# Optimization experiments

Measured on AMD Instinct MI355X. Metric: run time of the kernel, lower is better.

## Reference

```python
import jax, jax.numpy as jnp
import numpy as np
from jax import lax


def _lstm(x, W_ih, W_hh, b_ih, b_hh, return_seq):
    """PyTorch-compatible single-layer LSTM, batch_first, zero init state.
    W_ih: [4H, D], W_hh: [4H, H], gate order (i, f, g, o).
    Returns [B, T, H] if return_seq else final hidden [B, H]."""
    B, T, _ = x.shape
    H = W_hh.shape[1]
    # Precompute input contribution for all timesteps: [B, T, 4H]
    xg = jnp.einsum('btd,gd->btg', x, W_ih) + b_ih + b_hh
    h0 = jnp.zeros((B, H), x.dtype)
    c0 = jnp.zeros((B, H), x.dtype)

    def step(carry, xt):
        h, c = carry
        g = xt + h @ W_hh.T  # [B, 4H]
        i, f, gg, o = jnp.split(g, 4, axis=-1)
        i = jax.nn.sigmoid(i)
        f = jax.nn.sigmoid(f)
        gg = jnp.tanh(gg)
        o = jax.nn.sigmoid(o)
        c = f * c + i * gg
        h = o * jnp.tanh(c)
        return (h, c), (h if return_seq else None)

    (hT, _), ys = lax.scan(step, (h0, c0), jnp.swapaxes(xg, 0, 1))
    if return_seq:
        return jnp.swapaxes(ys, 0, 1)  # [B, T, H]
    return hT


def setup_inputs() -> dict:
    key = jax.random.key(0)
    ks = jax.random.split(key, 12)
    B, T, D = 2048, 512, 64
    H1, H2 = 16, 4
    s = 0.1
    return {
        'x': jax.random.normal(ks[0], (B, T, D), jnp.float32),
        'W_ih1': jax.random.normal(ks[1], (4 * H1, D), jnp.float32) * s,
        'W_hh1': jax.random.normal(ks[2], (4 * H1, H1), jnp.float32) * s,
        'b_ih1': jax.random.normal(ks[3], (4 * H1,), jnp.float32) * s,
        'b_hh1': jax.random.normal(ks[4], (4 * H1,), jnp.float32) * s,
        'W_ih2': jax.random.normal(ks[5], (4 * H2, H1), jnp.float32) * s,
        'W_hh2': jax.random.normal(ks[6], (4 * H2, H2), jnp.float32) * s,
        'b_ih2': jax.random.normal(ks[7], (4 * H2,), jnp.float32) * s,
        'b_hh2': jax.random.normal(ks[8], (4 * H2,), jnp.float32) * s,
        'W_fc': jax.random.normal(ks[9], (D, H2), jnp.float32) * s,
        'b_fc': jax.random.normal(ks[10], (D,), jnp.float32) * s,
    }


def reference(x, W_ih1, W_hh1, b_ih1, b_hh1, W_ih2, W_hh2, b_ih2, b_hh2, W_fc, b_fc):
    y = _lstm(x, W_ih1, W_hh1, b_ih1, b_hh1, return_seq=True)  # [B, T, H1]
    y = jax.nn.relu(y)
    # Only the last timestep of lstm2 is used -> return final hidden state.
    y_last = _lstm(y, W_ih2, W_hh2, b_ih2, b_hh2, return_seq=False)  # [B, H2]
    out = y_last @ W_fc.T + b_fc  # [B, D]
    return jax.nn.sigmoid(out)
```

## Files before the change

kernel.cpp:

```cpp
#include <hip/hip_runtime.h>
#include <hip/hip_bf16.h>

#define T_ALL 512
#define TB 16
#define NB (T_ALL / TB)
#define LOG2E 1.44269504088896f
#define XSTR 68

typedef __attribute__((ext_vector_type(8))) short bf16x8;
typedef __attribute__((ext_vector_type(4))) float f32x4;

#define DPPF(v, CTRL) __uint_as_float((unsigned)__builtin_amdgcn_update_dpp(0, (int)__float_as_uint(v), (CTRL), 0xF, 0xF, true))
#define SWZF(v, PAT)  __uint_as_float((unsigned)__builtin_amdgcn_ds_swizzle((int)__float_as_uint(v), (PAT)))
#define BPERM(a, v)   __uint_as_float((unsigned)__builtin_amdgcn_ds_bpermute((a), (int)__float_as_uint(v)))

__device__ __forceinline__ unsigned pack2bf16(float a, float b) {
    unsigned ua = __float_as_uint(a), ub = __float_as_uint(b);
    ua += 0x7FFFu + ((ua >> 16) & 1u);
    ub += 0x7FFFu + ((ub >> 16) & 1u);
    return (ua >> 16) | (ub & 0xFFFF0000u);
}
__device__ __forceinline__ bf16x8 make_frag(float4 lo, float4 hi) {
    union { unsigned u[4]; bf16x8 v; } r;
    r.u[0] = pack2bf16(lo.x, lo.y);
    r.u[1] = pack2bf16(lo.z, lo.w);
    r.u[2] = pack2bf16(hi.x, hi.y);
    r.u[3] = pack2bf16(hi.z, hi.w);
    return r.v;
}
__device__ __forceinline__ float4 scale4(float4 v, float s) {
    return make_float4(v.x * s, v.y * s, v.z * s, v.w * s);
}
__device__ __forceinline__ float2 pkfma(float2 a, float2 b, float2 c) {
    return make_float2(fmaf(a.x, b.x, c.x), fmaf(a.y, b.y, c.y));
}
__device__ __forceinline__ float tanh_c(float c) {
    return fmaf(2.0f, __builtin_amdgcn_rcpf(
        1.0f + __builtin_amdgcn_exp2f(-2.0f * LOG2E * c)), -1.0f);
}
__device__ __forceinline__ float fsigm(float x) {
    return __builtin_amdgcn_rcpf(1.0f + __builtin_amdgcn_exp2f(-LOG2E * x));
}

__global__ __launch_bounds__(128, 4)
void lstm_fused_v8(const float* __restrict__ x,
        const float* __restrict__ Wih1, const float* __restrict__ Whh1,
        const float* __restrict__ bih1, const float* __restrict__ bhh1,
        const float* __restrict__ Wih2, const float* __restrict__ Whh2,
        const float* __restrict__ bih2, const float* __restrict__ bhh2,
        const float* __restrict__ Wfc,  const float* __restrict__ bfc,
        float* __restrict__ out)
{
    __shared__ __align__(16) float xgl[2][TB * XSTR];
    __shared__ __align__(16) float h1l[2][TB][16];

    const int tid = threadIdx.x;
    const int wid = tid >> 6;
    const int lane = tid & 63;
    const size_t b = blockIdx.x;

    const int tl = lane & 15;
    const int kh = lane >> 4;
    const int T1 = lane & 3;
    const int j1 = lane >> 2;

    const float aA1 = (T1 == 2) ? 2.0f : 1.0f, aB1 = (T1 == 2) ? -1.0f : 0.0f;

    bf16x8 wb[4][2];
    float bias1[4];
#pragma unroll
    for (int n = 0; n < 4; ++n) {
        const float scn = (n == 2) ? 2.0f * LOG2E : LOG2E;
#pragma unroll
        for (int kk = 0; kk < 2; ++kk) {
            const float* wp = Wih1 + (size_t)(n * 16 + tl) * 64 + kk * 32 + kh * 8;
            wb[n][kk] = make_frag(scale4(*(const float4*)wp, scn),
                                  scale4(*(const float4*)(wp + 4), scn));
        }
        bias1[n] = (bih1[n * 16 + tl] + bhh1[n * 16 + tl]) * scn;
    }

    float2 wrA0, wrA1, wrB0, wrB1, wrC0, wrC1, wrD0, wrD1;
    {
        const float sA = (T1 == 2) ? 2.0f * LOG2E : LOG2E;
        const float sB = ((T1 ^ 2) == 2) ? 2.0f * LOG2E : LOG2E;
        const float sC = ((T1 ^ 1) == 2) ? 2.0f * LOG2E : LOG2E;
        const float sD = ((T1 ^ 3) == 2) ? 2.0f * LOG2E : LOG2E;
        const float4 wa  = scale4(*(const float4*)(Whh1 + ((T1    ) * 16 + j1) * 16 + 4 * T1), sA);
        const float4 wbv = scale4(*(const float4*)(Whh1 + ((T1 ^ 2) * 16 + j1) * 16 + 4 * T1), sB);
        const float4 wc  = scale4(*(const float4*)(Whh1 + ((T1 ^ 1) * 16 + j1) * 16 + 4 * T1), sC);
        const float4 wd  = scale4(*(const float4*)(Whh1 + ((T1 ^ 3) * 16 + j1) * 16 + 4 * T1), sD);
        wrA0 = make_float2(wa.x, wa.y);   wrA1 = make_float2(wa.z, wa.w);
        wrB0 = make_float2(wbv.x, wbv.y); wrB1 = make_float2(wbv.z, wbv.w);
        wrC0 = make_float2(wc.x, wc.y);   wrC1 = make_float2(wc.z, wc.w);
        wrD0 = make_float2(wd.x, wd.y);   wrD1 = make_float2(wd.z, wd.w);
    }

    const int m2 = lane >> 4;
    const int T2 = (lane >> 2) & 3;
    const int s2 = lane & 3;
    const int row2 = T2 * 4 + m2;
    const float sc2 = (T2 == 2) ? 2.0f * LOG2E : LOG2E;
    const float aA2 = (T2 == 2) ? 2.0f : 1.0f, aB2 = (T2 == 2) ? -1.0f : 0.0f;
    const float4 w2q = scale4(*(const float4*)(Wih2 + row2 * 16 + 4 * s2), sc2);
    const float2 w2a = make_float2(w2q.x, w2q.y);
    const float2 w2b = make_float2(w2q.z, w2q.w);
    const float w2h = Whh2[row2 * 4 + s2] * sc2;
    const float bias2l = (s2 == 0) ? (bih2[row2] + bhh2[row2]) * sc2 : 0.0f;
    const float4 wfc = *(const float4*)(Wfc + lane * 4);
    const float bfcv = bfc[lane];

    const int ag0 = (16 * T1 + 0)  << 2;
    const int ag1 = (16 * T1 + 4)  << 2;
    const int ag2 = (16 * T1 + 8)  << 2;
    const int ag3 = (16 * T1 + 12) << 2;
    const int ahs = s2 << 6;
    const int gidx = T1 * 16 + j1;

    float c1r = 0.f, h1r = 0.f;
    float c2r = 0.f, h2v = 0.f, h2s = 0.f;

    const float* xb = x + b * (size_t)(T_ALL * 64);
    float4 xpf[4];
    const float2 zero2 = make_float2(0.f, 0.f);

#define LOADX(CH) do { \
    const float* _src = xb + (size_t)(CH) * (TB * 64); \
    _Pragma("unroll") \
    for (int _kk = 0; _kk < 2; ++_kk) \
        _Pragma("unroll") \
        for (int _hf = 0; _hf < 2; ++_hf) \
            xpf[_kk * 2 + _hf] = *(const float4*)(_src + tl * 64 + _kk * 32 + kh * 8 + _hf * 4); \
} while (0)

#define MFMA_XG(BUF) do { \
    bf16x8 _a0 = make_frag(xpf[0], xpf[1]); \
    bf16x8 _a1 = make_frag(xpf[2], xpf[3]); \
    _Pragma("unroll") \
    for (int _n = 0; _n < 4; ++_n) { \
        f32x4 _acc = {bias1[_n], bias1[_n], bias1[_n], bias1[_n]}; \
        _acc = __builtin_amdgcn_mfma_f32_16x16x32_bf16(_a0, wb[_n][0], _acc, 0, 0, 0); \
        _acc = __builtin_amdgcn_mfma_f32_16x16x32_bf16(_a1, wb[_n][1], _acc, 0, 0, 0); \
        _Pragma("unroll") \
        for (int _r = 0; _r < 4; ++_r) \
            xgl[BUF][(kh * 4 + _r) * XSTR + _n * 16 + tl] = _acc[_r]; \
    } \
} while (0)

#define STEP1(XU) do { \
    const float _g0 = BPERM(ag0, h1r); \
    const float _g1 = BPERM(ag1, h1r); \
    const float _g2 = BPERM(ag2, h1r); \
    const float _g3 = BPERM(ag3, h1r); \
    const float2 _g01 = make_float2(_g0, _g1); \
    const float2 _g23 = make_float2(_g2, _g3); \
    float2 _aA = pkfma(wrA0, _g01, make_float2((XU), 0.f)); _aA = pkfma(wrA1, _g23, _aA); \
    float2 _aB = pkfma(wrB0, _g01, zero2); _aB = pkfma(wrB1, _g23, _aB); \
    float2 _aC = pkfma(wrC0, _g01, zero2); _aC = pkfma(wrC1, _g23, _aC); \
    float2 _aD = pkfma(wrD0, _g01, zero2); _aD = pkfma(wrD1, _g23, _aD); \
    const float _sA = _aA.x + _aA.y, _sB2 = _aB.x + _aB.y; \
    const float _sC = _aC.x + _aC.y, _sD = _aD.x + _aD.y; \
    const float _u0 = _sA + DPPF(_sC, 0xB1); \
    const float _u1 = _sB2 + DPPF(_sD, 0xB1); \
    const float _pre = _u0 + DPPF(_u1, 0x4E); \
    const float _s1 = __builtin_amdgcn_rcpf(1.0f + __builtin_amdgcn_exp2f(-_pre)); \
    const float _act = fmaf(aA1, _s1, aB1); \
    const float _fv = DPPF(_act, 0x55); \
    const float _gv = DPPF(_act, 0xAA); \
    const float _ov = DPPF(_act, 0xFF); \
    c1r = fmaf(_fv, c1r, _act * _gv);         \
    h1r = _ov * tanh_c(c1r);                  \
} while (0)

#define LSTM2_STEP(RG, TT) do { \
    const float4 _rq = *(const float4*)&h1l[RG][TT][4 * s2]; \
    const float2 _r01 = make_float2(fmaxf(_rq.x, 0.f), fmaxf(_rq.y, 0.f)); \
    const float2 _r23 = make_float2(fmaxf(_rq.z, 0.f), fmaxf(_rq.w, 0.f)); \
    float2 _a2 = pkfma(w2a, _r01, make_float2(bias2l, w2h * h2s)); \
    _a2 = pkfma(w2b, _r23, _a2); \
    float _p2 = _a2.x + _a2.y; \
    _p2 += DPPF(_p2, 0xB1); \
    _p2 += DPPF(_p2, 0x4E); \
    const float _act2 = fmaf(aA2, \
        __builtin_amdgcn_rcpf(1.0f + __builtin_amdgcn_exp2f(-_p2)), aB2); \
    const float _fv2 = SWZF(_act2, 0x101F); \
    const float _gv2 = SWZF(_act2, 0x201F); \
    const float _ov2 = SWZF(_act2, 0x301F); \
    c2r = fmaf(_fv2, c2r, _act2 * _gv2);      \
    h2v = _ov2 * tanh_c(c2r); \
    h2s = BPERM(ahs, h2v); \
} while (0)

    if (wid == 1) {
        LOADX(0);
        MFMA_XG(0);
        LOADX(1);
    }
    __syncthreads();

    for (int c = 0; c < NB; ++c) {
        if (wid == 0) {
            const float* xrow = &xgl[c & 1][0];
            const int rg = c & 1;
#pragma unroll
            for (int tt = 0; tt < TB; ++tt) {
                const float xu = xrow[tt * XSTR + gidx];
                STEP1(xu);
                if (T1 == 0) h1l[rg][tt][j1] = h1r;
            }
        } else {
            if (c + 1 < NB) {
                bf16x8 a0s = make_frag(xpf[0], xpf[1]);
                bf16x8 a1s = make_frag(xpf[2], xpf[3]);
                if (c + 2 < NB) LOADX(c + 2);
#pragma unroll
                for (int n = 0; n < 4; ++n) {
                    f32x4 acc = {bias1[n], bias1[n], bias1[n], bias1[n]};
                    acc = __builtin_amdgcn_mfma_f32_16x16x32_bf16(a0s, wb[n][0], acc, 0, 0, 0);
                    acc = __builtin_amdgcn_mfma_f32_16x16x32_bf16(a1s, wb[n][1], acc, 0, 0, 0);
#pragma unroll
                    for (int r = 0; r < 4; ++r)
                        xgl[(c + 1) & 1][(kh * 4 + r) * XSTR + n * 16 + tl] = acc[r];
                }
            }
            if (c >= 1) {
                const int rg = (c - 1) & 1;
#pragma unroll
                for (int tt = 0; tt < TB; ++tt)
                    LSTM2_STEP(rg, tt);
            }
        }
        __syncthreads();
    }

    if (wid == 1) {
        const int rg = (NB - 1) & 1;
#pragma unroll
        for (int tt = 0; tt < TB; ++tt)
            LSTM2_STEP(rg, tt);

        const float hq0 = __shfl(h2v, 0);
        const float hq1 = __shfl(h2v, 16);
        const float hq2 = __shfl(h2v, 32);
        const float hq3 = __shfl(h2v, 48);
        float accf = bfcv;
        accf = fmaf(wfc.x, hq0, accf);
        accf = fmaf(wfc.y, hq1, accf);
        accf = fmaf(wfc.z, hq2, accf);
        accf = fmaf(wfc.w, hq3, accf);
        out[b * 64 + lane] = fsigm(accf);
    }
#undef LOADX
#undef MFMA_XG
#undef STEP1
#undef LSTM2_STEP
}

extern "C" void kernel_launch(void* const* d_in, const int* in_sizes, int n_in,
                              void* d_out, int out_size, void* d_ws, size_t ws_size,
                              hipStream_t stream) {
    const float* x    = (const float*)d_in[0];
    const float* Wih1 = (const float*)d_in[1];
    const float* Whh1 = (const float*)d_in[2];
    const float* bih1 = (const float*)d_in[3];
    const float* bhh1 = (const float*)d_in[4];
    const float* Wih2 = (const float*)d_in[5];
    const float* Whh2 = (const float*)d_in[6];
    const float* bih2 = (const float*)d_in[7];
    const float* bhh2 = (const float*)d_in[8];
    const float* Wfc  = (const float*)d_in[9];
    const float* bfc  = (const float*)d_in[10];
    float* out = (float*)d_out;

    lstm_fused_v8<<<dim3(2048), dim3(128), 0, stream>>>(
        x, Wih1, Whh1, bih1, bhh1, Wih2, Whh2, bih2, bhh2, Wfc, bfc, out);
}
```

Before: 161.3 us.

## Batch LSTM2 input projection per chunk with MFMA, trim recurrent critical path

The layer-2 input projection (ReLU(h1) times Wih2 plus bias) moves out of the per-timestep loop. Each 16-step chunk now computes it with one bf16 MFMA into a shared buffer, so each LSTM2 step only does the recurrent term plus a shared-memory load. The layer-1 step adds the precomputed input term after the DPP reductions, taking it off the dependent FMA chain. The bf16 packing switches from round-to-nearest-even to a cheaper add-and-perm rounding, and layer-2 input weights and activations are now rounded to bf16, which costs some precision.

```diff
diff --git a/kernel.cpp b/kernel.cpp
--- a/kernel.cpp
+++ b/kernel.cpp
@@ -14,25 +14,30 @@
 #define SWZF(v, PAT)  __uint_as_float((unsigned)__builtin_amdgcn_ds_swizzle((int)__float_as_uint(v), (PAT)))
 #define BPERM(a, v)   __uint_as_float((unsigned)__builtin_amdgcn_ds_bpermute((a), (int)__float_as_uint(v)))
 
-__device__ __forceinline__ unsigned pack2bf16(float a, float b) {
-    unsigned ua = __float_as_uint(a), ub = __float_as_uint(b);
-    ua += 0x7FFFu + ((ua >> 16) & 1u);
-    ub += 0x7FFFu + ((ub >> 16) & 1u);
-    return (ua >> 16) | (ub & 0xFFFF0000u);
+__device__ __forceinline__ unsigned pack2fast(float a, float b) {
+    const unsigned ua = __float_as_uint(a) + 0x8000u;
+    const unsigned ub = __float_as_uint(b) + 0x8000u;
+    return __builtin_amdgcn_perm(ub, ua, 0x07060302u);
 }
 __device__ __forceinline__ bf16x8 make_frag(float4 lo, float4 hi) {
     union { unsigned u[4]; bf16x8 v; } r;
-    r.u[0] = pack2bf16(lo.x, lo.y);
-    r.u[1] = pack2bf16(lo.z, lo.w);
-    r.u[2] = pack2bf16(hi.x, hi.y);
-    r.u[3] = pack2bf16(hi.z, hi.w);
+    r.u[0] = pack2fast(lo.x, lo.y);
+    r.u[1] = pack2fast(lo.z, lo.w);
+    r.u[2] = pack2fast(hi.x, hi.y);
+    r.u[3] = pack2fast(hi.z, hi.w);
     return r.v;
 }
 __device__ __forceinline__ float4 scale4(float4 v, float s) {
     return make_float4(v.x * s, v.y * s, v.z * s, v.w * s);
 }
+__device__ __forceinline__ float4 relu4(float4 v) {
+    return make_float4(fmaxf(v.x, 0.f), fmaxf(v.y, 0.f), fmaxf(v.z, 0.f), fmaxf(v.w, 0.f));
+}
 __device__ __forceinline__ float2 pkfma(float2 a, float2 b, float2 c) {
     return make_float2(fmaf(a.x, b.x, c.x), fmaf(a.y, b.y, c.y));
+}
+__device__ __forceinline__ float2 pkmul(float2 a, float2 b) {
+    return make_float2(a.x * b.x, a.y * b.y);
 }
 __device__ __forceinline__ float tanh_c(float c) {
     return fmaf(2.0f, __builtin_amdgcn_rcpf(
@@ -43,7 +48,7 @@
 }
 
 __global__ __launch_bounds__(128, 4)
-void lstm_fused_v8(const float* __restrict__ x,
+void lstm_fused_v9(const float* __restrict__ x,
         const float* __restrict__ Wih1, const float* __restrict__ Whh1,
         const float* __restrict__ bih1, const float* __restrict__ bhh1,
         const float* __restrict__ Wih2, const float* __restrict__ Whh2,
@@ -53,6 +58,7 @@
 {
     __shared__ __align__(16) float xgl[2][TB * XSTR];
     __shared__ __align__(16) float h1l[2][TB][16];
+    __shared__ __align__(16) float xg2l[TB * 16];
 
     const int tid = threadIdx.x;
     const int wid = tid >> 6;
@@ -96,17 +102,32 @@
         wrD0 = make_float2(wd.x, wd.y);   wrD1 = make_float2(wd.z, wd.w);
     }
 
+    bf16x8 wA2;
+    {
+        union { unsigned u[4]; bf16x8 v; } z;
+        z.u[0] = z.u[1] = z.u[2] = z.u[3] = 0u;
+        wA2 = z.v;
+        if (kh < 2) {
+            const float scr = ((tl >> 2) == 2) ? 2.0f * LOG2E : LOG2E;
+            const float* wp = Wih2 + tl * 16 + kh * 8;
+            wA2 = make_frag(scale4(*(const float4*)wp, scr),
+                            scale4(*(const float4*)(wp + 4), scr));
+        }
+    }
+    f32x4 bias2v;
+#pragma unroll
+    for (int r = 0; r < 4; ++r) {
+        const int g = 4 * kh + r;
+        bias2v[r] = (bih2[g] + bhh2[g]) * (((g >> 2) == 2) ? 2.0f * LOG2E : LOG2E);
+    }
+
     const int m2 = lane >> 4;
     const int T2 = (lane >> 2) & 3;
     const int s2 = lane & 3;
     const int row2 = T2 * 4 + m2;
     const float sc2 = (T2 == 2) ? 2.0f * LOG2E : LOG2E;
     const float aA2 = (T2 == 2) ? 2.0f : 1.0f, aB2 = (T2 == 2) ? -1.0f : 0.0f;
-    const float4 w2q = scale4(*(const float4*)(Wih2 + row2 * 16 + 4 * s2), sc2);
-    const float2 w2a = make_float2(w2q.x, w2q.y);
-    const float2 w2b = make_float2(w2q.z, w2q.w);
     const float w2h = Whh2[row2 * 4 + s2] * sc2;
-    const float bias2l = (s2 == 0) ? (bih2[row2] + bhh2[row2]) * sc2 : 0.0f;
     const float4 wfc = *(const float4*)(Wfc + lane * 4);
     const float bfcv = bfc[lane];
 
@@ -122,7 +143,6 @@
 
     const float* xb = x + b * (size_t)(T_ALL * 64);
     float4 xpf[4];
-    const float2 zero2 = make_float2(0.f, 0.f);
 
 #define LOADX(CH) do { \
     const float* _src = xb + (size_t)(CH) * (TB * 64); \
@@ -133,20 +153,6 @@
             xpf[_kk * 2 + _hf] = *(const float4*)(_src + tl * 64 + _kk * 32 + kh * 8 + _hf * 4); \
 } while (0)
 
-#define MFMA_XG(BUF) do { \
-    bf16x8 _a0 = make_frag(xpf[0], xpf[1]); \
-    bf16x8 _a1 = make_frag(xpf[2], xpf[3]); \
-    _Pragma("unroll") \
-    for (int _n = 0; _n < 4; ++_n) { \
-        f32x4 _acc = {bias1[_n], bias1[_n], bias1[_n], bias1[_n]}; \
-        _acc = __builtin_amdgcn_mfma_f32_16x16x32_bf16(_a0, wb[_n][0], _acc, 0, 0, 0); \
-        _acc = __builtin_amdgcn_mfma_f32_16x16x32_bf16(_a1, wb[_n][1], _acc, 0, 0, 0); \
-        _Pragma("unroll") \
-        for (int _r = 0; _r < 4; ++_r) \
-            xgl[BUF][(kh * 4 + _r) * XSTR + _n * 16 + tl] = _acc[_r]; \
-    } \
-} while (0)
-
 #define STEP1(XU) do { \
     const float _g0 = BPERM(ag0, h1r); \
     const float _g1 = BPERM(ag1, h1r); \
@@ -154,15 +160,15 @@
     const float _g3 = BPERM(ag3, h1r); \
     const float2 _g01 = make_float2(_g0, _g1); \
     const float2 _g23 = make_float2(_g2, _g3); \
-    float2 _aA = pkfma(wrA0, _g01, make_float2((XU), 0.f)); _aA = pkfma(wrA1, _g23, _aA); \
-    float2 _aB = pkfma(wrB0, _g01, zero2); _aB = pkfma(wrB1, _g23, _aB); \
-    float2 _aC = pkfma(wrC0, _g01, zero2); _aC = pkfma(wrC1, _g23, _aC); \
-    float2 _aD = pkfma(wrD0, _g01, zero2); _aD = pkfma(wrD1, _g23, _aD); \
+    float2 _aA = pkmul(wrA0, _g01); _aA = pkfma(wrA1, _g23, _aA); \
+    float2 _aB = pkmul(wrB0, _g01); _aB = pkfma(wrB1, _g23, _aB); \
+    float2 _aC = pkmul(wrC0, _g01); _aC = pkfma(wrC1, _g23, _aC); \
+    float2 _aD = pkmul(wrD0, _g01); _aD = pkfma(wrD1, _g23, _aD); \
     const float _sA = _aA.x + _aA.y, _sB2 = _aB.x + _aB.y; \
     const float _sC = _aC.x + _aC.y, _sD = _aD.x + _aD.y; \
     const float _u0 = _sA + DPPF(_sC, 0xB1); \
     const float _u1 = _sB2 + DPPF(_sD, 0xB1); \
-    const float _pre = _u0 + DPPF(_u1, 0x4E); \
+    const float _pre = _u0 + DPPF(_u1, 0x4E) + (XU); \
     const float _s1 = __builtin_amdgcn_rcpf(1.0f + __builtin_amdgcn_exp2f(-_pre)); \
     const float _act = fmaf(aA1, _s1, aB1); \
     const float _fv = DPPF(_act, 0x55); \
@@ -172,15 +178,27 @@
     h1r = _ov * tanh_c(c1r);                  \
 } while (0)
 
-#define LSTM2_STEP(RG, TT) do { \
-    const float4 _rq = *(const float4*)&h1l[RG][TT][4 * s2]; \
-    const float2 _r01 = make_float2(fmaxf(_rq.x, 0.f), fmaxf(_rq.y, 0.f)); \
-    const float2 _r23 = make_float2(fmaxf(_rq.z, 0.f), fmaxf(_rq.w, 0.f)); \
-    float2 _a2 = pkfma(w2a, _r01, make_float2(bias2l, w2h * h2s)); \
-    _a2 = pkfma(w2b, _r23, _a2); \
-    float _p2 = _a2.x + _a2.y; \
+#define GATES2(RG) do { \
+    bf16x8 _bf; \
+    { union { unsigned u[4]; bf16x8 v; } _z; _z.u[0]=_z.u[1]=_z.u[2]=_z.u[3]=0u; _bf = _z.v; } \
+    if (kh < 2) { \
+        const float4 _h0 = *(const float4*)&h1l[RG][tl][8 * kh]; \
+        const float4 _h1 = *(const float4*)&h1l[RG][tl][8 * kh + 4]; \
+        _bf = make_frag(relu4(_h0), relu4(_h1)); \
+    } \
+    f32x4 _acc = bias2v; \
+    _acc = __builtin_amdgcn_mfma_f32_16x16x32_bf16(wA2, _bf, _acc, 0, 0, 0); \
+    _Pragma("unroll") \
+    for (int _r = 0; _r < 4; ++_r) \
+        xg2l[tl * 16 + 4 * kh + _r] = _acc[_r]; \
+} while (0)
+
+#define LSTM2_STEP(TT) do { \
+    const float _xg2 = xg2l[(TT) * 16 + row2]; \
+    float _p2 = w2h * h2s; \
     _p2 += DPPF(_p2, 0xB1); \
     _p2 += DPPF(_p2, 0x4E); \
+    _p2 += _xg2; \
     const float _act2 = fmaf(aA2, \
         __builtin_amdgcn_rcpf(1.0f + __builtin_amdgcn_exp2f(-_p2)), aB2); \
     const float _fv2 = SWZF(_act2, 0x101F); \
@@ -193,7 +211,19 @@
 
     if (wid == 1) {
         LOADX(0);
-        MFMA_XG(0);
+        {
+            bf16x8 a0s = make_frag(xpf[0], xpf[1]);
+            bf16x8 a1s = make_frag(xpf[2], xpf[3]);
+#pragma unroll
+            for (int n = 0; n < 4; ++n) {
+                f32x4 acc = {bias1[n], bias1[n], bias1[n], bias1[n]};
+                acc = __builtin_amdgcn_mfma_f32_16x16x32_bf16(a0s, wb[n][0], acc, 0, 0, 0);
+                acc = __builtin_amdgcn_mfma_f32_16x16x32_bf16(a1s, wb[n][1], acc, 0, 0, 0);
+#pragma unroll
+                for (int r = 0; r < 4; ++r)
+                    xgl[0][(kh * 4 + r) * XSTR + n * 16 + tl] = acc[r];
+            }
+        }
         LOADX(1);
     }
     __syncthreads();
@@ -224,20 +254,20 @@
                 }
             }
             if (c >= 1) {
-                const int rg = (c - 1) & 1;
+                GATES2((c - 1) & 1);
 #pragma unroll
                 for (int tt = 0; tt < TB; ++tt)
-                    LSTM2_STEP(rg, tt);
+                    LSTM2_STEP(tt);
             }
         }
         __syncthreads();
     }
 
     if (wid == 1) {
-        const int rg = (NB - 1) & 1;
+        GATES2((NB - 1) & 1);
 #pragma unroll
         for (int tt = 0; tt < TB; ++tt)
-            LSTM2_STEP(rg, tt);
+            LSTM2_STEP(tt);
 
         const float hq0 = __shfl(h2v, 0);
         const float hq1 = __shfl(h2v, 16);
@@ -251,8 +281,8 @@
         out[b * 64 + lane] = fsigm(accf);
     }
 #undef LOADX
-#undef MFMA_XG
 #undef STEP1
+#undef GATES2
 #undef LSTM2_STEP
 }
 
@@ -272,6 +302,6 @@
     const float* bfc  = (const float*)d_in[10];
     float* out = (float*)d_out;
 
-    lstm_fused_v8<<<dim3(2048), dim3(128), 0, stream>>>(
+    lstm_fused_v9<<<dim3(2048), dim3(128), 0, stream>>>(
         x, Wih1, Whh1, bih1, bhh1, Wih2, Whh2, bih2, bhh2, Wfc, bfc, out);
 }
```

After: 161.7 us. About the same (+0.3%).
